# Performance work log

Measured on AMD Instinct MI355X. Metric: run time of the kernel, lower is better.

The kernel has to match this reference:

```python
import jax, jax.numpy as jnp
import numpy as np

B, M, N = 4, 1024, 32768

def setup_inputs() -> dict:
    key = jax.random.key(0)
    k1, k2 = jax.random.split(key)
    keypoints = jax.random.normal(k1, (B, 3, M), dtype=jnp.float32)
    pc = jax.random.normal(k2, (B, 3, N), dtype=jnp.float32)
    return {"keypoints": keypoints, "pc": pc}

def reference(keypoints, pc):
    # Pairwise Euclidean distances via the expanded quadratic form:
    # ||k - p||^2 = ||k||^2 + ||p||^2 - 2 k.p  -> avoids the [B,3,M,N] tensor.
    k2 = jnp.sum(keypoints * keypoints, axis=1)            # [B, M]
    p2 = jnp.sum(pc * pc, axis=1)                          # [B, N]
    cross = jnp.einsum("bdm,bdn->bmn", keypoints, pc)     # [B, M, N]
    d2 = k2[:, :, None] + p2[:, None, :] - 2.0 * cross     # [B, M, N]
    dist = jnp.sqrt(jnp.maximum(d2, 0.0))
    min_dist = jnp.min(dist, axis=2)                       # [B, M]
    return jnp.mean(min_dist)
```

## Files before the change

kernel.cpp:

```cpp
#include <hip/hip_runtime.h>
#include <math.h>

#define BATCH 4
#define M 1024
#define N 32768
#define NSPLIT 256
#define CHUNK (N / NSPLIT)
#define TPB 256
#define KPT 4
#define ROWS (BATCH * M)

#define K2_BLOCKS 64
#define K2_TPB 256
#define K2_ROWS (ROWS / K2_BLOCKS)

#define BSUM_OFF (NSPLIT * ROWS)

__global__ __launch_bounds__(TPB) void p2p_partial(
        const float* __restrict__ kp, const float* __restrict__ pc,
        float* __restrict__ pws) {
    __shared__ __align__(16) float px[CHUNK];
    __shared__ __align__(16) float py[CHUNK];
    __shared__ __align__(16) float pz[CHUNK];
    __shared__ __align__(16) float pw[CHUNK];

    const int b = blockIdx.x / NSPLIT;
    const int c = blockIdx.x % NSPLIT;
    const int t = threadIdx.x;

    const float* pcb = pc + (size_t)b * 3 * N + c * CHUNK;
    if (t < CHUNK) {
        float x = pcb[t], y = pcb[N + t], z = pcb[2 * N + t];
        px[t] = x; py[t] = y; pz[t] = z;
        pw[t] = -0.5f * fmaf(x, x, fmaf(y, y, z * z));
    }

    const float* kpb = kp + (size_t)b * 3 * M;
    float kx[KPT], ky[KPT], kz[KPT], k2[KPT], mq[KPT];
#pragma unroll
    for (int k = 0; k < KPT; ++k) {
        int m = t + k * TPB;
        kx[k] = kpb[m];
        ky[k] = kpb[M + m];
        kz[k] = kpb[2 * M + m];
        k2[k] = fmaf(kx[k], kx[k], fmaf(ky[k], ky[k], kz[k] * kz[k]));
        mq[k] = -INFINITY;
    }
    __syncthreads();

#pragma unroll 2
    for (int j = 0; j < CHUNK; j += 4) {
        float4 vx = *(const float4*)&px[j];
        float4 vy = *(const float4*)&py[j];
        float4 vz = *(const float4*)&pz[j];
        float4 vw = *(const float4*)&pw[j];
        float X[4] = {vx.x, vx.y, vx.z, vx.w};
        float Y[4] = {vy.x, vy.y, vy.z, vy.w};
        float Z[4] = {vz.x, vz.y, vz.z, vz.w};
        float W[4] = {vw.x, vw.y, vw.z, vw.w};
#pragma unroll
        for (int k = 0; k < KPT; ++k) {
            float q0 = fmaf(kz[k], Z[0], fmaf(ky[k], Y[0], fmaf(kx[k], X[0], W[0])));
            float q1 = fmaf(kz[k], Z[1], fmaf(ky[k], Y[1], fmaf(kx[k], X[1], W[1])));
            float q2 = fmaf(kz[k], Z[2], fmaf(ky[k], Y[2], fmaf(kx[k], X[2], W[2])));
            float q3 = fmaf(kz[k], Z[3], fmaf(ky[k], Y[3], fmaf(kx[k], X[3], W[3])));
            mq[k] = fmaxf(fmaxf(mq[k], q0), q1);
            mq[k] = fmaxf(fmaxf(mq[k], q2), q3);
        }
    }

    float* dst = pws + (size_t)c * ROWS + b * M;
#pragma unroll
    for (int k = 0; k < KPT; ++k) {
        float d2 = fmaxf(fmaf(-2.0f, mq[k], k2[k]), 0.0f);
        dst[t + k * TPB] = d2;
    }
}

__global__ __launch_bounds__(K2_TPB) void p2p_colmin(
        const float* __restrict__ pws, float* __restrict__ bsum) {
    __shared__ float smin[4][K2_ROWS];
    const int t = threadIdx.x;
    const int r = t & 63;
    const int g = t >> 6;
    const int row = blockIdx.x * K2_ROWS + r;

    float v = INFINITY;
#pragma unroll 8
    for (int ci = 0; ci < NSPLIT / 4; ++ci) {
        int c = g * (NSPLIT / 4) + ci;
        v = fminf(v, pws[(size_t)c * ROWS + row]);
    }
    smin[g][r] = v;
    __syncthreads();

    if (t < 64) {
        float m = fminf(fminf(smin[0][t], smin[1][t]),
                        fminf(smin[2][t], smin[3][t]));
        float s = sqrtf(m);
#pragma unroll
        for (int off = 32; off > 0; off >>= 1) s += __shfl_down(s, off, 64);
        if (t == 0) bsum[blockIdx.x] = s;
    }
}

__global__ __launch_bounds__(64) void p2p_final(
        const float* __restrict__ bsum, float* __restrict__ out) {
    const int t = threadIdx.x;
    float s = bsum[t];
#pragma unroll
    for (int off = 32; off > 0; off >>= 1) s += __shfl_down(s, off, 64);
    if (t == 0) out[0] = s / (float)ROWS;
}

extern "C" void kernel_launch(void* const* d_in, const int* in_sizes, int n_in,
                              void* d_out, int out_size, void* d_ws, size_t ws_size,
                              hipStream_t stream) {
    const float* kp = (const float*)d_in[0];
    const float* pc = (const float*)d_in[1];
    float* out = (float*)d_out;
    float* pws = (float*)d_ws;

    p2p_partial<<<BATCH * NSPLIT, TPB, 0, stream>>>(kp, pc, pws);
    p2p_colmin<<<K2_BLOCKS, K2_TPB, 0, stream>>>(pws, pws + BSUM_OFF);
    p2p_final<<<1, 64, 0, stream>>>(pws + BSUM_OFF, out);
}
```

Baseline: 81.25 us.

## Broadcast points via readlane instead of LDS and fold final reduction into colmin

Each wavefront now loads its own 128 points into registers and broadcasts them with readlane, removing the shared-memory staging and the block barrier. The final mean is folded into the column-min kernel through a last-block ticket counter, which drops one kernel launch. Launch bounds are also tightened to request higher occupancy. Readlane goes through scalar registers and may serialize on the SALU/VALU path, and each wavefront now fetches the point chunk redundantly from global memory.

```diff
diff --git a/kernel.cpp b/kernel.cpp
--- a/kernel.cpp
+++ b/kernel.cpp
@@ -15,25 +15,28 @@
 #define K2_ROWS (ROWS / K2_BLOCKS)
 
 #define BSUM_OFF (NSPLIT * ROWS)
+#define TICKET_OFF (BSUM_OFF + K2_BLOCKS)
 
-__global__ __launch_bounds__(TPB) void p2p_partial(
+__device__ __forceinline__ float rlane(float v, int u) {
+    return __int_as_float(__builtin_amdgcn_readlane(__float_as_int(v), u));
+}
+
+__global__ __launch_bounds__(TPB, 4) void p2p_partial(
         const float* __restrict__ kp, const float* __restrict__ pc,
         float* __restrict__ pws) {
-    __shared__ __align__(16) float px[CHUNK];
-    __shared__ __align__(16) float py[CHUNK];
-    __shared__ __align__(16) float pz[CHUNK];
-    __shared__ __align__(16) float pw[CHUNK];
-
     const int b = blockIdx.x / NSPLIT;
     const int c = blockIdx.x % NSPLIT;
     const int t = threadIdx.x;
+    const int l = t & 63;
+
+    if (blockIdx.x == 0 && t == 0)
+        ((unsigned*)pws)[TICKET_OFF] = 0u;
 
     const float* pcb = pc + (size_t)b * 3 * N + c * CHUNK;
-    if (t < CHUNK) {
-        float x = pcb[t], y = pcb[N + t], z = pcb[2 * N + t];
-        px[t] = x; py[t] = y; pz[t] = z;
-        pw[t] = -0.5f * fmaf(x, x, fmaf(y, y, z * z));
-    }
+    float x0 = pcb[l],      y0 = pcb[N + l],      z0 = pcb[2 * N + l];
+    float x1 = pcb[64 + l], y1 = pcb[N + 64 + l], z1 = pcb[2 * N + 64 + l];
+    float w0 = -0.5f * fmaf(x0, x0, fmaf(y0, y0, z0 * z0));
+    float w1 = -0.5f * fmaf(x1, x1, fmaf(y1, y1, z1 * z1));
 
     const float* kpb = kp + (size_t)b * 3 * M;
     float kx[KPT], ky[KPT], kz[KPT], k2[KPT], mq[KPT];
@@ -46,26 +49,31 @@
         k2[k] = fmaf(kx[k], kx[k], fmaf(ky[k], ky[k], kz[k] * kz[k]));
         mq[k] = -INFINITY;
     }
-    __syncthreads();
 
-#pragma unroll 2
-    for (int j = 0; j < CHUNK; j += 4) {
-        float4 vx = *(const float4*)&px[j];
-        float4 vy = *(const float4*)&py[j];
-        float4 vz = *(const float4*)&pz[j];
-        float4 vw = *(const float4*)&pw[j];
-        float X[4] = {vx.x, vx.y, vx.z, vx.w};
-        float Y[4] = {vy.x, vy.y, vy.z, vy.w};
-        float Z[4] = {vz.x, vz.y, vz.z, vz.w};
-        float W[4] = {vw.x, vw.y, vw.z, vw.w};
+#pragma unroll 8
+    for (int u = 0; u < 64; u += 2) {
+        float Xa = rlane(x0, u),     Ya = rlane(y0, u);
+        float Za = rlane(z0, u),     Wa = rlane(w0, u);
+        float Xb = rlane(x0, u + 1), Yb = rlane(y0, u + 1);
+        float Zb = rlane(z0, u + 1), Wb = rlane(w0, u + 1);
 #pragma unroll
         for (int k = 0; k < KPT; ++k) {
-            float q0 = fmaf(kz[k], Z[0], fmaf(ky[k], Y[0], fmaf(kx[k], X[0], W[0])));
-            float q1 = fmaf(kz[k], Z[1], fmaf(ky[k], Y[1], fmaf(kx[k], X[1], W[1])));
-            float q2 = fmaf(kz[k], Z[2], fmaf(ky[k], Y[2], fmaf(kx[k], X[2], W[2])));
-            float q3 = fmaf(kz[k], Z[3], fmaf(ky[k], Y[3], fmaf(kx[k], X[3], W[3])));
-            mq[k] = fmaxf(fmaxf(mq[k], q0), q1);
-            mq[k] = fmaxf(fmaxf(mq[k], q2), q3);
+            float qa = fmaf(kx[k], Xa, fmaf(ky[k], Ya, fmaf(kz[k], Za, Wa)));
+            float qb = fmaf(kx[k], Xb, fmaf(ky[k], Yb, fmaf(kz[k], Zb, Wb)));
+            mq[k] = fmaxf(fmaxf(mq[k], qa), qb);
+        }
+    }
+#pragma unroll 8
+    for (int u = 0; u < 64; u += 2) {
+        float Xa = rlane(x1, u),     Ya = rlane(y1, u);
+        float Za = rlane(z1, u),     Wa = rlane(w1, u);
+        float Xb = rlane(x1, u + 1), Yb = rlane(y1, u + 1);
+        float Zb = rlane(z1, u + 1), Wb = rlane(w1, u + 1);
+#pragma unroll
+        for (int k = 0; k < KPT; ++k) {
+            float qa = fmaf(kx[k], Xa, fmaf(ky[k], Ya, fmaf(kz[k], Za, Wa)));
+            float qb = fmaf(kx[k], Xb, fmaf(ky[k], Yb, fmaf(kz[k], Zb, Wb)));
+            mq[k] = fmaxf(fmaxf(mq[k], qa), qb);
         }
     }
 
@@ -78,8 +86,10 @@
 }
 
 __global__ __launch_bounds__(K2_TPB) void p2p_colmin(
-        const float* __restrict__ pws, float* __restrict__ bsum) {
+        const float* __restrict__ pws, float* __restrict__ bsum,
+        unsigned* __restrict__ ticket, float* __restrict__ out) {
     __shared__ float smin[4][K2_ROWS];
+    __shared__ int lastflag;
     const int t = threadIdx.x;
     const int r = t & 63;
     const int g = t >> 6;
@@ -100,17 +110,21 @@
         float s = sqrtf(m);
 #pragma unroll
         for (int off = 32; off > 0; off >>= 1) s += __shfl_down(s, off, 64);
-        if (t == 0) bsum[blockIdx.x] = s;
+        if (t == 0) {
+            bsum[blockIdx.x] = s;
+            __threadfence();
+            unsigned tk = atomicAdd(ticket, 1u);
+            lastflag = (tk == K2_BLOCKS - 1) ? 1 : 0;
+        }
     }
-}
-
-__global__ __launch_bounds__(64) void p2p_final(
-        const float* __restrict__ bsum, float* __restrict__ out) {
-    const int t = threadIdx.x;
-    float s = bsum[t];
+    __syncthreads();
+    if (lastflag && t < 64) {
+        float s = __hip_atomic_load(&bsum[t], __ATOMIC_RELAXED,
+                                    __HIP_MEMORY_SCOPE_AGENT);
 #pragma unroll
-    for (int off = 32; off > 0; off >>= 1) s += __shfl_down(s, off, 64);
-    if (t == 0) out[0] = s / (float)ROWS;
+        for (int off = 32; off > 0; off >>= 1) s += __shfl_down(s, off, 64);
+        if (t == 0) out[0] = s / (float)ROWS;
+    }
 }
 
 extern "C" void kernel_launch(void* const* d_in, const int* in_sizes, int n_in,
@@ -122,6 +136,6 @@
     float* pws = (float*)d_ws;
 
     p2p_partial<<<BATCH * NSPLIT, TPB, 0, stream>>>(kp, pc, pws);
-    p2p_colmin<<<K2_BLOCKS, K2_TPB, 0, stream>>>(pws, pws + BSUM_OFF);
-    p2p_final<<<1, 64, 0, stream>>>(pws + BSUM_OFF, out);
+    p2p_colmin<<<K2_BLOCKS, K2_TPB, 0, stream>>>(
+        pws, pws + BSUM_OFF, (unsigned*)(pws + TICKET_OFF), out);
 }
```

Measured after the change: 93.31 us. 1.15x slower.
